# Kernel optimization log

Measured on AMD Instinct MI355X. Metric: run time of the kernel, lower is better.

## Reference

```python
import jax, jax.numpy as jnp
import numpy as np

N_NODES = 100000
N_EDGES = 1250000
D = 64
L = 2  # number of conv layers (len(hid_ds) - 1)
BN_EPS = 1e-5


def setup_inputs() -> dict:
    key = jax.random.key(0)
    ks = jax.random.split(key, 16)
    s = 1.0 / np.sqrt(D)
    inp = {
        "x": jax.random.normal(ks[0], (N_NODES, D), dtype=jnp.float32),
        "edge_index": jax.random.randint(ks[1], (2, N_EDGES), 0, N_NODES, dtype=jnp.int32),
        "batch": jnp.zeros((N_NODES,), dtype=jnp.int32),
        # stacked per-layer parameters [L, D, D] / [L, D]
        "Wk": jax.random.uniform(ks[2], (L, D, D), jnp.float32, -s, s),
        "bk": jax.random.uniform(ks[3], (L, D), jnp.float32, -s, s),
        "Wq": jax.random.uniform(ks[4], (L, D, D), jnp.float32, -s, s),
        "bq": jax.random.uniform(ks[5], (L, D), jnp.float32, -s, s),
        "Wv": jax.random.uniform(ks[6], (L, D, D), jnp.float32, -s, s),
        "bv": jax.random.uniform(ks[7], (L, D), jnp.float32, -s, s),
        "Ws": jax.random.uniform(ks[8], (L, D, D), jnp.float32, -s, s),
        "bs": jax.random.uniform(ks[9], (L, D), jnp.float32, -s, s),
        "bias": jnp.zeros((L, D), dtype=jnp.float32),
        "gamma": jnp.ones((L, D), dtype=jnp.float32),
        "beta": jnp.zeros((L, D), dtype=jnp.float32),
    }
    return inp


def _res_gated_conv(x, src, dst, Wk, bk, Wq, bq, Wv, bv, Ws, bs, b):
    # per-node linear transforms (dense GEMMs on [N, D])
    k = x @ Wk + bk          # applied at target i
    q = x @ Wq + bq          # applied at source j
    v = x @ Wv + bv          # message value from source j
    # edge-wise gather -> gate -> message: [E, D]
    msg = jax.nn.sigmoid(k[dst] + q[src]) * v[src]
    # scatter-add aggregation to targets
    agg = jnp.zeros_like(k).at[dst].add(msg)
    return agg + x @ Ws + bs + b


def _batch_norm(x, gamma, beta):
    # training-mode BatchNorm1d over node axis, biased variance
    mean = jnp.mean(x, axis=0)
    var = jnp.mean(jnp.square(x - mean), axis=0)
    return (x - mean) * jax.lax.rsqrt(var + BN_EPS) * gamma + beta


def reference(x, edge_index, batch, Wk, bk, Wq, bq, Wv, bv, Ws, bs, bias, gamma, beta):
    src = edge_index[0]  # source j
    dst = edge_index[1]  # target i
    for l in range(L):
        x = _res_gated_conv(x, src, dst, Wk[l], bk[l], Wq[l], bq[l],
                            Wv[l], bv[l], Ws[l], bs[l], bias[l])
        x = jax.nn.relu(x)
        x = _batch_norm(x, gamma[l], beta[l])
    return x
```

## Files before the change

### kernel.cpp

```cpp
#include <hip/hip_runtime.h>
#include <math.h>

#define D 64
#define BN_EPS 1e-5f
#define CH 160
#define BSH 7
#define BCAP 8192
#define NBLK 256

using short8 = __attribute__((ext_vector_type(8))) short;
using f32x4  = __attribute__((ext_vector_type(4))) float;

static __device__ __forceinline__ unsigned short f2bf(float f) {
    unsigned int u = __float_as_uint(f);
    unsigned int r = (u + 0x7fffu + ((u >> 16) & 1u)) >> 16;
    return (unsigned short)r;
}
static __device__ __forceinline__ float bf2f(unsigned short u) {
    return __uint_as_float(((unsigned int)u) << 16);
}
static __device__ __forceinline__ float clamp60(float x) {
    return fminf(fmaxf(x, -60.f), 60.f);
}

__global__ __launch_bounds__(256) void prep_weights(
    const float* __restrict__ Wk, const float* __restrict__ Wq,
    const float* __restrict__ Wv, const float* __restrict__ Ws,
    unsigned short* __restrict__ Wfrag)
{
    int idx = blockIdx.x * 256 + threadIdx.x;
    int i    = idx & 7;
    int lane = (idx >> 3) & 63;
    int kb   = (idx >> 9) & 1;
    int nc   = (idx >> 10) & 3;
    int m    = (idx >> 12) & 3;
    int l    = (idx >> 14) & 1;
    int k = kb * 32 + (lane >> 4) * 8 + i;
    int n = nc * 16 + (lane & 15);
    const float* W = (m == 0) ? Wk : (m == 1) ? Wq : (m == 2) ? Wv : Ws;
    Wfrag[idx] = f2bf(W[(size_t)l * 4096 + k * 64 + n]);
}

template<bool APPLY_BN>
__global__ __launch_bounds__(256) void gemm_fused(
    const float* x,
    const unsigned short* __restrict__ Wfrag,
    const float* __restrict__ bk, const float* __restrict__ bq,
    const float* __restrict__ bv, const float* __restrict__ bs,
    const float* __restrict__ bias, const float* __restrict__ stats,
    unsigned short* __restrict__ EKh, unsigned int* __restrict__ QV,
    float* AGG, int nrows)
{
    __shared__ unsigned short xt[64 * 64];
    const int t = threadIdx.x;
    const int row0 = blockIdx.x * 64;

    #pragma unroll
    for (int it = 0; it < 4; ++it) {
        int fidx = t + it * 256;
        int r = fidx >> 4, c4 = fidx & 15;
        int grow = row0 + r;
        float4 v = make_float4(0.f, 0.f, 0.f, 0.f);
        if (grow < nrows)
            v = *reinterpret_cast<const float4*>(&x[(size_t)grow * D + c4 * 4]);
        if (APPLY_BN) {
            const float4* st4 = reinterpret_cast<const float4*>(stats);
            float4 sc = st4[32 + c4], sh = st4[48 + c4];
            v.x = fmaxf(v.x, 0.f) * sc.x + sh.x;
            v.y = fmaxf(v.y, 0.f) * sc.y + sh.y;
            v.z = fmaxf(v.z, 0.f) * sc.z + sh.z;
            v.w = fmaxf(v.w, 0.f) * sc.w + sh.w;
        }
        ushort4 b;
        b.x = f2bf(v.x); b.y = f2bf(v.y); b.z = f2bf(v.z); b.w = f2bf(v.w);
        int phys = (c4 >> 1) ^ (r & 7);
        *reinterpret_cast<ushort4*>(&xt[r * 64 + phys * 8 + (c4 & 1) * 4]) = b;
    }
    __syncthreads();

    const int w = t >> 6, lane = t & 63;
    const int rbase = w * 16;

    short8 A[2];
    #pragma unroll
    for (int kb = 0; kb < 2; ++kb) {
        int r = rbase + (lane & 15);
        int c16 = (kb * 4 + (lane >> 4)) ^ (r & 7);
        A[kb] = *reinterpret_cast<const short8*>(&xt[r * 64 + c16 * 8]);
    }

    f32x4 acc[4][4];
    #pragma unroll
    for (int m = 0; m < 4; ++m)
        #pragma unroll
        for (int nc = 0; nc < 4; ++nc)
            acc[m][nc] = (f32x4){0.f, 0.f, 0.f, 0.f};

    #pragma unroll
    for (int nc = 0; nc < 4; ++nc) {
        #pragma unroll
        for (int m = 0; m < 4; ++m) {
            #pragma unroll
            for (int kb = 0; kb < 2; ++kb) {
                short8 B = *reinterpret_cast<const short8*>(
                    &Wfrag[((((m * 4 + nc) * 2 + kb) * 64) + lane) * 8]);
                acc[m][nc] = __builtin_amdgcn_mfma_f32_16x16x32_bf16(A[kb], B, acc[m][nc], 0, 0, 0);
            }
        }
    }

    const int crow = rbase + ((lane >> 4) << 2);
    #pragma unroll
    for (int nc = 0; nc < 4; ++nc) {
        int c = nc * 16 + (lane & 15);
        float bkc = bk[c], bqc = bq[c], bvc = bv[c], bsc = bs[c] + bias[c];
        #pragma unroll
        for (int reg = 0; reg < 4; ++reg) {
            int grow = row0 + crow + reg;
            if (grow < nrows) {
                size_t o = (size_t)grow * D + c;
                EKh[o] = f2bf(__expf(-clamp60(acc[0][nc][reg] + bkc)));
                float eq = __expf(-clamp60(acc[1][nc][reg] + bqc));
                QV[o] = ((unsigned int)f2bf(acc[2][nc][reg] + bvc) << 16) | (unsigned int)f2bf(eq);
                AGG[o] = acc[3][nc][reg] + bsc;
            }
        }
    }
}

__global__ __launch_bounds__(256) void bin_count(const int* __restrict__ dst,
                                                 int* __restrict__ cnt,
                                                 int nedges, int NB)
{
    __shared__ int h[1024];
    const int t = threadIdx.x, b = blockIdx.x;
    for (int i = t; i < NB; i += 256) h[i] = 0;
    __syncthreads();
    const int e0 = (int)(((long long)nedges * b) / NBLK);
    const int e1 = (int)(((long long)nedges * (b + 1)) / NBLK);
    for (int i = e0 + t; i < e1; i += 256)
        atomicAdd(&h[dst[i] >> BSH], 1);
    __syncthreads();
    for (int i = t; i < NB; i += 256) cnt[b * NB + i] = h[i];
}

__global__ __launch_bounds__(256) void scan_mat(const int* __restrict__ cnt,
                                                int* __restrict__ basel,
                                                int* __restrict__ btot, int NB)
{
    __shared__ int tmp[256];
    const int k = blockIdx.x;
    const int t = threadIdx.x;
    int v = cnt[t * NB + k];
    tmp[t] = v;
    __syncthreads();
    for (int off = 1; off < 256; off <<= 1) {
        int add = (t >= off) ? tmp[t - off] : 0;
        __syncthreads();
        tmp[t] += add;
        __syncthreads();
    }
    basel[t * NB + k] = tmp[t] - v;
    if (t == 255) btot[k] = tmp[255];
}

__global__ __launch_bounds__(1024) void scan_buckets(const int* __restrict__ btot,
                                                     int* __restrict__ boff,
                                                     float* __restrict__ stats,
                                                     int* __restrict__ offs,
                                                     int NB, int n, int nedges)
{
    __shared__ int tmp[1024];
    const int t = threadIdx.x;
    int v = (t < NB) ? btot[t] : 0;
    tmp[t] = v;
    __syncthreads();
    for (int off = 1; off < 1024; off <<= 1) {
        int add = (t >= off) ? tmp[t - off] : 0;
        __syncthreads();
        tmp[t] += add;
        __syncthreads();
    }
    if (t < NB) boff[t] = tmp[t] - v;
    if (t < 128) stats[t] = 0.f;
    if (t == 0) offs[n] = nedges;
}

__global__ __launch_bounds__(256) void bin_emit(const int* __restrict__ src,
                                                const int* __restrict__ dst,
                                                const int* __restrict__ basel,
                                                const int* __restrict__ boff,
                                                unsigned int* __restrict__ bin,
                                                int nedges, int NB)
{
    __shared__ int cur[1024];
    const int t = threadIdx.x, b = blockIdx.x;
    for (int i = t; i < NB; i += 256) cur[i] = boff[i] + basel[b * NB + i];
    __syncthreads();
    const int e0 = (int)(((long long)nedges * b) / NBLK);
    const int e1 = (int)(((long long)nedges * (b + 1)) / NBLK);
    for (int i = e0 + t; i < e1; i += 256) {
        int d = dst[i];
        int pos = atomicAdd(&cur[d >> BSH], 1);
        bin[pos] = ((unsigned int)src[i] << BSH) | (unsigned int)(d & ((1 << BSH) - 1));
    }
}

__global__ __launch_bounds__(256) void bucket_csr(const unsigned int* __restrict__ bin,
                                                  const int* __restrict__ boff,
                                                  const int* __restrict__ btot,
                                                  int* __restrict__ offs,
                                                  int* __restrict__ csr_src, int n)
{
    __shared__ unsigned int lsrc[BCAP];
    __shared__ int ldeg[128], loff[128], lcur[128];
    const int t = threadIdx.x;
    const int b = blockIdx.x;
    const int base = boff[b];
    const int cnt  = btot[b];

    if (t < 128) ldeg[t] = 0;
    __syncthreads();
    for (int j = t; j < cnt; j += 256)
        atomicAdd(&ldeg[bin[base + j] & ((1 << BSH) - 1)], 1);
    __syncthreads();
    if (t < 128) loff[t] = ldeg[t];
    __syncthreads();
    for (int off = 1; off < 128; off <<= 1) {
        int add = (t < 128 && t >= off) ? loff[t - off] : 0;
        __syncthreads();
        if (t < 128) loff[t] += add;
        __syncthreads();
    }
    if (t < 128) {
        int ex = loff[t] - ldeg[t];
        lcur[t] = ex;
        int node = (b << BSH) + t;
        if (node < n) offs[node] = base + ex;
    }
    __syncthreads();
    for (int j = t; j < cnt; j += 256) {
        unsigned int e = bin[base + j];
        int pos = atomicAdd(&lcur[e & ((1 << BSH) - 1)], 1);
        lsrc[pos] = e >> BSH;
    }
    __syncthreads();
    for (int j = t; j < cnt; j += 256)
        csr_src[base + j] = (int)lsrc[j];
}

__global__ __launch_bounds__(256) void nstart_bs(const int* __restrict__ offs,
                                                 int* __restrict__ node_start,
                                                 int n, int NC)
{
    int c = blockIdx.x * 256 + threadIdx.x;
    if (c >= NC) return;
    int target = c * CH;
    int a = 0, bnd = n;
    while (a < bnd) {
        int mid = (a + bnd) >> 1;
        if (offs[mid + 1] > target) bnd = mid; else a = mid + 1;
    }
    node_start[c] = a;
}

__global__ __launch_bounds__(256) void edge_agg(
    const int* __restrict__ csr_src, const int* __restrict__ offs,
    const int* __restrict__ node_start,
    const unsigned short* __restrict__ EKh, const unsigned int* __restrict__ QV,
    float* __restrict__ AGG, int nnodes)
{
    const int lane  = threadIdx.x & 63;
    const int chunk = __builtin_amdgcn_readfirstlane((int)((blockIdx.x * 256 + threadIdx.x) >> 6));
    const int Etot  = offs[nnodes];
    const int e0 = chunk * CH;
    if (e0 >= Etot) return;
    const int e1 = min(e0 + CH, Etot);

    int n      = node_start[chunk];
    int nstart = offs[n];
    int nend   = offs[n + 1];

    float acc = 0.f;
    float ek  = bf2f(EKh[((size_t)n << 6) | lane]);

    auto flush = [&](bool partial) {
        int idx = (n << 6) | lane;
        if (partial) atomicAdd(&AGG[idx], acc);
        else         AGG[idx] += acc;
    };
    auto advance = [&](int eidx) {
        do { ++n; } while (offs[n + 1] == eidx);
        nstart = eidx;
        nend   = offs[n + 1];
        acc = 0.f;
        ek  = bf2f(EKh[((size_t)n << 6) | lane]);
    };

    for (int e = e0; e < e1; e += 64) {
        const int cnt = min(64, e1 - e);
        int sAll = (lane < cnt) ? csr_src[e + lane] : 0;
        for (int b = 0; b < cnt; b += 16) {
            const int bc = min(16, cnt - b);
            unsigned int p[16];
            #pragma unroll
            for (int u = 0; u < 16; ++u) {
                if (u < bc) {
                    int s = __shfl(sAll, b + u);
                    p[u] = QV[((size_t)s << 6) | lane];
                }
            }
            #pragma unroll
            for (int u = 0; u < 16; ++u) {
                if (u < bc) {
                    int eidx = e + b + u;
                    if (eidx == nend) { flush(nstart < e0); advance(eidx); }
                    float eq = __uint_as_float(p[u] << 16);
                    float vv = __uint_as_float(p[u] & 0xffff0000u);
                    float g  = __builtin_amdgcn_rcpf(fmaf(ek, eq, 1.0f));
                    acc = fmaf(g, vv, acc);
                }
            }
        }
    }
    flush((nstart < e0) || (nend > e1));
}

__global__ __launch_bounds__(256) void relu_stats(
    const float* __restrict__ AGG, float* __restrict__ stats, int n4)
{
    __shared__ float ls[128];
    const int t = threadIdx.x;
    if (t < 128) ls[t] = 0.f;
    __syncthreads();
    int idx = blockIdx.x * 256 + t;
    const int stride = gridDim.x * 256;
    const int f0 = (idx << 2) & 63;
    float s0=0,s1=0,s2=0,s3=0,q0=0,q1=0,q2=0,q3=0;
    for (; idx < n4; idx += stride) {
        float4 a = reinterpret_cast<const float4*>(AGG)[idx];
        a.x = fmaxf(a.x, 0.f); a.y = fmaxf(a.y, 0.f);
        a.z = fmaxf(a.z, 0.f); a.w = fmaxf(a.w, 0.f);
        s0 += a.x; q0 = fmaf(a.x, a.x, q0);
        s1 += a.y; q1 = fmaf(a.y, a.y, q1);
        s2 += a.z; q2 = fmaf(a.z, a.z, q2);
        s3 += a.w; q3 = fmaf(a.w, a.w, q3);
    }
    atomicAdd(&ls[f0],     s0); atomicAdd(&ls[f0 + 1],     s1);
    atomicAdd(&ls[f0 + 2], s2); atomicAdd(&ls[f0 + 3],     s3);
    atomicAdd(&ls[64 + f0],     q0); atomicAdd(&ls[64 + f0 + 1], q1);
    atomicAdd(&ls[64 + f0 + 2], q2); atomicAdd(&ls[64 + f0 + 3], q3);
    __syncthreads();
    if (t < 128) atomicAdd(&stats[t], ls[t]);
}

__global__ void finalize_stats(float* __restrict__ stats,
                               const float* __restrict__ gamma,
                               const float* __restrict__ beta, int nrows)
{
    int t = threadIdx.x;
    float invN = 1.0f / (float)nrows;
    float mean = stats[t] * invN;
    float var  = stats[64 + t] * invN - mean * mean;
    float sc   = gamma[t] * rsqrtf(var + BN_EPS);
    stats[128 + t] = sc;
    stats[192 + t] = beta[t] - mean * sc;
    stats[t] = 0.f;
    stats[64 + t] = 0.f;
}

__global__ __launch_bounds__(256) void apply_bn(
    const float* __restrict__ AGG, const float* __restrict__ stats,
    float* __restrict__ xout, int ntot4)
{
    int idx = blockIdx.x * 256 + threadIdx.x;
    const int stride = gridDim.x * 256;
    const float4* st4 = reinterpret_cast<const float4*>(stats);
    for (; idx < ntot4; idx += stride) {
        float4 a = reinterpret_cast<const float4*>(AGG)[idx];
        int c4 = idx & 15;
        float4 sc = st4[32 + c4];
        float4 sh = st4[48 + c4];
        float4 o;
        o.x = fmaxf(a.x, 0.f) * sc.x + sh.x;
        o.y = fmaxf(a.y, 0.f) * sc.y + sh.y;
        o.z = fmaxf(a.z, 0.f) * sc.z + sh.z;
        o.w = fmaxf(a.w, 0.f) * sc.w + sh.w;
        reinterpret_cast<float4*>(xout)[idx] = o;
    }
}

extern "C" void kernel_launch(void* const* d_in, const int* in_sizes, int n_in,
                              void* d_out, int out_size, void* d_ws, size_t ws_size,
                              hipStream_t stream)
{
    const float* x     = (const float*)d_in[0];
    const int*   ei    = (const int*)d_in[1];
    const float* Wk    = (const float*)d_in[3];
    const float* bk    = (const float*)d_in[4];
    const float* Wq    = (const float*)d_in[5];
    const float* bq    = (const float*)d_in[6];
    const float* Wv    = (const float*)d_in[7];
    const float* bv    = (const float*)d_in[8];
    const float* Ws    = (const float*)d_in[9];
    const float* bs    = (const float*)d_in[10];
    const float* bias  = (const float*)d_in[11];
    const float* gamma = (const float*)d_in[12];
    const float* beta  = (const float*)d_in[13];

    const int nrows  = in_sizes[0] / D;
    const int nedges = in_sizes[1] / 2;
    const int nm     = nrows * D;
    const int NB     = (nrows + (1 << BSH) - 1) >> BSH;
    const int NC     = (nedges + CH - 1) / CH;

    float* out = (float*)d_out;
    float* ws  = (float*)d_ws;
    unsigned short* EKh = (unsigned short*)ws;
    unsigned int* QV = (unsigned int*)(EKh + nm);
    float* AGG = (float*)(QV + nm);
    float* stats = AGG + nm;
    int* offs    = (int*)(stats + 256);
    unsigned int* bin = (unsigned int*)(offs + nrows + 1);
    int* csr_src = (int*)(bin + nedges);
    int* cnt     = csr_src + nedges;
    int* basel   = cnt + NBLK * NB;
    int* btot    = basel + NBLK * NB;
    int* boff    = btot + NB;
    int* nstart_map = boff + NB;
    unsigned short* Wfrag = (unsigned short*)(nstart_map + NC);

    const int* srcI = ei;
    const int* dstI = ei + nedges;

    const int gemm_blocks = (nrows + 63) / 64;
    const int agg_blocks  = (NC + 3) / 4;

    prep_weights<<<128, 256, 0, stream>>>(Wk, Wq, Wv, Ws, Wfrag);
    bin_count<<<NBLK, 256, 0, stream>>>(dstI, cnt, nedges, NB);
    scan_mat<<<NB, 256, 0, stream>>>(cnt, basel, btot, NB);
    scan_buckets<<<1, 1024, 0, stream>>>(btot, boff, stats, offs, NB, nrows, nedges);
    bin_emit<<<NBLK, 256, 0, stream>>>(srcI, dstI, basel, boff, bin, nedges, NB);
    bucket_csr<<<NB, 256, 0, stream>>>(bin, boff, btot, offs, csr_src, nrows);
    nstart_bs<<<(NC + 255) / 256, 256, 0, stream>>>(offs, nstart_map, nrows, NC);

    gemm_fused<false><<<gemm_blocks, 256, 0, stream>>>(x, Wfrag,
        bk, bq, bv, bs, bias, stats, EKh, QV, AGG, nrows);
    edge_agg<<<agg_blocks, 256, 0, stream>>>(csr_src, offs, nstart_map, EKh, QV, AGG, nrows);
    relu_stats<<<1024, 256, 0, stream>>>(AGG, stats, nm / 4);
    finalize_stats<<<1, 64, 0, stream>>>(stats, gamma, beta, nrows);

    gemm_fused<true><<<gemm_blocks, 256, 0, stream>>>(AGG, Wfrag + 16384,
        bk + D, bq + D, bv + D, bs + D, bias + D, stats, EKh, QV, AGG, nrows);
    edge_agg<<<agg_blocks, 256, 0, stream>>>(csr_src, offs, nstart_map, EKh, QV, AGG, nrows);
    relu_stats<<<1024, 256, 0, stream>>>(AGG, stats, nm / 4);
    finalize_stats<<<1, 64, 0, stream>>>(stats, gamma + D, beta + D, nrows);
    apply_bn<<<2048, 256, 0, stream>>>(AGG, stats, out, nm / 4);
}
```

Baseline: 339.7 us.

## Fuse BN statistics into edge aggregation and fold finalize into consumers

Removes the separate relu_stats pass over AGG by accumulating ReLU sum and sum-of-squares in edge_agg when a node's row is fully owned by a wave. A new cleanup_stats kernel picks up nodes finished via atomics or with no incoming edges. The finalize_stats kernel is dropped: the next GEMM and apply_bn recompute scale and shift into shared memory. This saves a full read of AGG and a launch per layer, but adds cleanup logic and extra global atomics whose correctness depends on subtle chunk-boundary ownership.

```diff
diff --git a/kernel.cpp b/kernel.cpp
--- a/kernel.cpp
+++ b/kernel.cpp
@@ -48,12 +48,26 @@
     const float* __restrict__ bk, const float* __restrict__ bq,
     const float* __restrict__ bv, const float* __restrict__ bs,
     const float* __restrict__ bias, const float* __restrict__ stats,
+    const float* __restrict__ gamma, const float* __restrict__ beta,
     unsigned short* __restrict__ EKh, unsigned int* __restrict__ QV,
     float* AGG, int nrows)
 {
     __shared__ unsigned short xt[64 * 64];
+    __shared__ float scsh[128];
     const int t = threadIdx.x;
     const int row0 = blockIdx.x * 64;
+
+    if (APPLY_BN) {
+        if (t < 64) {
+            float invN = 1.0f / (float)nrows;
+            float mean = stats[t] * invN;
+            float var  = stats[64 + t] * invN - mean * mean;
+            float sc   = gamma[t] * rsqrtf(var + BN_EPS);
+            scsh[t] = sc;
+            scsh[64 + t] = beta[t] - mean * sc;
+        }
+        __syncthreads();
+    }
 
     #pragma unroll
     for (int it = 0; it < 4; ++it) {
@@ -64,8 +78,8 @@
         if (grow < nrows)
             v = *reinterpret_cast<const float4*>(&x[(size_t)grow * D + c4 * 4]);
         if (APPLY_BN) {
-            const float4* st4 = reinterpret_cast<const float4*>(stats);
-            float4 sc = st4[32 + c4], sh = st4[48 + c4];
+            float4 sc = reinterpret_cast<const float4*>(scsh)[c4];
+            float4 sh = reinterpret_cast<const float4*>(scsh)[16 + c4];
             v.x = fmaxf(v.x, 0.f) * sc.x + sh.x;
             v.y = fmaxf(v.y, 0.f) * sc.y + sh.y;
             v.z = fmaxf(v.z, 0.f) * sc.z + sh.z;
@@ -182,7 +196,7 @@
         __syncthreads();
     }
     if (t < NB) boff[t] = tmp[t] - v;
-    if (t < 128) stats[t] = 0.f;
+    if (t < 256) stats[t] = 0.f;
     if (t == 0) offs[n] = nedges;
 }
 
@@ -268,119 +282,153 @@
     const int* __restrict__ csr_src, const int* __restrict__ offs,
     const int* __restrict__ node_start,
     const unsigned short* __restrict__ EKh, const unsigned int* __restrict__ QV,
-    float* __restrict__ AGG, int nnodes)
-{
-    const int lane  = threadIdx.x & 63;
-    const int chunk = __builtin_amdgcn_readfirstlane((int)((blockIdx.x * 256 + threadIdx.x) >> 6));
+    float* __restrict__ AGG, float* __restrict__ stats, int nnodes)
+{
+    const int t = threadIdx.x;
+    const int lane  = t & 63;
+    const int chunk = __builtin_amdgcn_readfirstlane((int)((blockIdx.x * 256 + t) >> 6));
     const int Etot  = offs[nnodes];
     const int e0 = chunk * CH;
-    if (e0 >= Etot) return;
-    const int e1 = min(e0 + CH, Etot);
-
-    int n      = node_start[chunk];
-    int nstart = offs[n];
-    int nend   = offs[n + 1];
-
-    float acc = 0.f;
-    float ek  = bf2f(EKh[((size_t)n << 6) | lane]);
-
-    auto flush = [&](bool partial) {
-        int idx = (n << 6) | lane;
-        if (partial) atomicAdd(&AGG[idx], acc);
-        else         AGG[idx] += acc;
-    };
-    auto advance = [&](int eidx) {
-        do { ++n; } while (offs[n + 1] == eidx);
-        nstart = eidx;
-        nend   = offs[n + 1];
-        acc = 0.f;
-        ek  = bf2f(EKh[((size_t)n << 6) | lane]);
-    };
-
-    for (int e = e0; e < e1; e += 64) {
-        const int cnt = min(64, e1 - e);
-        int sAll = (lane < cnt) ? csr_src[e + lane] : 0;
-        for (int b = 0; b < cnt; b += 16) {
-            const int bc = min(16, cnt - b);
-            unsigned int p[16];
-            #pragma unroll
-            for (int u = 0; u < 16; ++u) {
-                if (u < bc) {
-                    int s = __shfl(sAll, b + u);
-                    p[u] = QV[((size_t)s << 6) | lane];
+    float lsum = 0.f, lsq = 0.f;
+
+    if (e0 < Etot) {
+        const int e1 = min(e0 + CH, Etot);
+
+        int n      = node_start[chunk];
+        int nstart = offs[n];
+        int nend   = offs[n + 1];
+
+        float acc = 0.f;
+        float ek  = bf2f(EKh[((size_t)n << 6) | lane]);
+
+        auto flush = [&](bool partial) {
+            int idx = (n << 6) | lane;
+            if (partial) {
+                atomicAdd(&AGG[idx], acc);
+            } else {
+                float cur = AGG[idx] + acc;
+                AGG[idx] = cur;
+                float y = fmaxf(cur, 0.f);
+                lsum += y;
+                lsq = fmaf(y, y, lsq);
+            }
+        };
+        auto advance = [&](int eidx) {
+            do { ++n; } while (offs[n + 1] == eidx);
+            nstart = eidx;
+            nend   = offs[n + 1];
+            acc = 0.f;
+            ek  = bf2f(EKh[((size_t)n << 6) | lane]);
+        };
+
+        for (int e = e0; e < e1; e += 64) {
+            const int cnt = min(64, e1 - e);
+            int sAll = (lane < cnt) ? csr_src[e + lane] : 0;
+            for (int b = 0; b < cnt; b += 16) {
+                const int bc = min(16, cnt - b);
+                unsigned int p[16];
+                #pragma unroll
+                for (int u = 0; u < 16; ++u) {
+                    if (u < bc) {
+                        int s = __shfl(sAll, b + u);
+                        p[u] = QV[((size_t)s << 6) | lane];
+                    }
+                }
+                #pragma unroll
+                for (int u = 0; u < 16; ++u) {
+                    if (u < bc) {
+                        int eidx = e + b + u;
+                        if (eidx == nend) { flush(nstart < e0); advance(eidx); }
+                        float eq = __uint_as_float(p[u] << 16);
+                        float vv = __uint_as_float(p[u] & 0xffff0000u);
+                        float g  = __builtin_amdgcn_rcpf(fmaf(ek, eq, 1.0f));
+                        acc = fmaf(g, vv, acc);
+                    }
                 }
             }
-            #pragma unroll
-            for (int u = 0; u < 16; ++u) {
-                if (u < bc) {
-                    int eidx = e + b + u;
-                    if (eidx == nend) { flush(nstart < e0); advance(eidx); }
-                    float eq = __uint_as_float(p[u] << 16);
-                    float vv = __uint_as_float(p[u] & 0xffff0000u);
-                    float g  = __builtin_amdgcn_rcpf(fmaf(ek, eq, 1.0f));
-                    acc = fmaf(g, vv, acc);
-                }
+        }
+        flush((nstart < e0) || (nend > e1));
+    }
+
+    __shared__ float ss[256], sq2[256];
+    ss[t] = lsum; sq2[t] = lsq;
+    __syncthreads();
+    if (t < 64) {
+        float s4 = ss[t] + ss[t + 64] + ss[t + 128] + ss[t + 192];
+        float q4 = sq2[t] + sq2[t + 64] + sq2[t + 128] + sq2[t + 192];
+        if (s4 != 0.f) atomicAdd(&stats[t], s4);
+        if (q4 != 0.f) atomicAdd(&stats[64 + t], q4);
+    }
+}
+
+__global__ __launch_bounds__(256) void cleanup_stats(
+    const int* __restrict__ offs, const int* __restrict__ node_start,
+    const float* __restrict__ AGG, float* __restrict__ stats, int n, int NC)
+{
+    const int t = threadIdx.x;
+    const int lane = t & 63;
+    const int wave = (blockIdx.x * 256 + t) >> 6;
+    float lsum = 0.f, lsq = 0.f;
+
+    if (wave < NC) {
+        int c = wave;
+        if (c > 0) {
+            int nd = node_start[c];
+            int s = offs[nd];
+            if (s < c * CH && s >= (c - 1) * CH) {
+                float y = fmaxf(AGG[((size_t)nd << 6) | lane], 0.f);
+                lsum = y; lsq = y * y;
             }
         }
-    }
-    flush((nstart < e0) || (nend > e1));
-}
-
-__global__ __launch_bounds__(256) void relu_stats(
-    const float* __restrict__ AGG, float* __restrict__ stats, int n4)
-{
-    __shared__ float ls[128];
-    const int t = threadIdx.x;
-    if (t < 128) ls[t] = 0.f;
-    __syncthreads();
+    } else {
+        int base = (wave - NC) << 6;
+        int nd = base + lane;
+        bool empty = (nd < n) && (offs[nd + 1] == offs[nd]);
+        unsigned long long mask = __ballot(empty);
+        while (mask) {
+            int b = __ffsll((unsigned long long)mask) - 1;
+            mask &= mask - 1;
+            int nd2 = base + b;
+            float y = fmaxf(AGG[((size_t)nd2 << 6) | lane], 0.f);
+            lsum += y; lsq = fmaf(y, y, lsq);
+        }
+    }
+
+    __shared__ float ss[256], sq2[256];
+    ss[t] = lsum; sq2[t] = lsq;
+    __syncthreads();
+    if (t < 64) {
+        float s4 = ss[t] + ss[t + 64] + ss[t + 128] + ss[t + 192];
+        float q4 = sq2[t] + sq2[t + 64] + sq2[t + 128] + sq2[t + 192];
+        if (s4 != 0.f) atomicAdd(&stats[t], s4);
+        if (q4 != 0.f) atomicAdd(&stats[64 + t], q4);
+    }
+}
+
+__global__ __launch_bounds__(256) void apply_bn(
+    const float* __restrict__ AGG, const float* __restrict__ stats,
+    const float* __restrict__ gamma, const float* __restrict__ beta,
+    float* __restrict__ xout, int ntot4, int nrows)
+{
+    __shared__ float scsh[128];
+    const int t = threadIdx.x;
+    if (t < 64) {
+        float invN = 1.0f / (float)nrows;
+        float mean = stats[t] * invN;
+        float var  = stats[64 + t] * invN - mean * mean;
+        float sc   = gamma[t] * rsqrtf(var + BN_EPS);
+        scsh[t] = sc;
+        scsh[64 + t] = beta[t] - mean * sc;
+    }
+    __syncthreads();
+
     int idx = blockIdx.x * 256 + t;
     const int stride = gridDim.x * 256;
-    const int f0 = (idx << 2) & 63;
-    float s0=0,s1=0,s2=0,s3=0,q0=0,q1=0,q2=0,q3=0;
-    for (; idx < n4; idx += stride) {
-        float4 a = reinterpret_cast<const float4*>(AGG)[idx];
-        a.x = fmaxf(a.x, 0.f); a.y = fmaxf(a.y, 0.f);
-        a.z = fmaxf(a.z, 0.f); a.w = fmaxf(a.w, 0.f);
-        s0 += a.x; q0 = fmaf(a.x, a.x, q0);
-        s1 += a.y; q1 = fmaf(a.y, a.y, q1);
-        s2 += a.z; q2 = fmaf(a.z, a.z, q2);
-        s3 += a.w; q3 = fmaf(a.w, a.w, q3);
-    }
-    atomicAdd(&ls[f0],     s0); atomicAdd(&ls[f0 + 1],     s1);
-    atomicAdd(&ls[f0 + 2], s2); atomicAdd(&ls[f0 + 3],     s3);
-    atomicAdd(&ls[64 + f0],     q0); atomicAdd(&ls[64 + f0 + 1], q1);
-    atomicAdd(&ls[64 + f0 + 2], q2); atomicAdd(&ls[64 + f0 + 3], q3);
-    __syncthreads();
-    if (t < 128) atomicAdd(&stats[t], ls[t]);
-}
-
-__global__ void finalize_stats(float* __restrict__ stats,
-                               const float* __restrict__ gamma,
-                               const float* __restrict__ beta, int nrows)
-{
-    int t = threadIdx.x;
-    float invN = 1.0f / (float)nrows;
-    float mean = stats[t] * invN;
-    float var  = stats[64 + t] * invN - mean * mean;
-    float sc   = gamma[t] * rsqrtf(var + BN_EPS);
-    stats[128 + t] = sc;
-    stats[192 + t] = beta[t] - mean * sc;
-    stats[t] = 0.f;
-    stats[64 + t] = 0.f;
-}
-
-__global__ __launch_bounds__(256) void apply_bn(
-    const float* __restrict__ AGG, const float* __restrict__ stats,
-    float* __restrict__ xout, int ntot4)
-{
-    int idx = blockIdx.x * 256 + threadIdx.x;
-    const int stride = gridDim.x * 256;
-    const float4* st4 = reinterpret_cast<const float4*>(stats);
     for (; idx < ntot4; idx += stride) {
         float4 a = reinterpret_cast<const float4*>(AGG)[idx];
         int c4 = idx & 15;
-        float4 sc = st4[32 + c4];
-        float4 sh = st4[48 + c4];
+        float4 sc = reinterpret_cast<const float4*>(scsh)[c4];
+        float4 sh = reinterpret_cast<const float4*>(scsh)[16 + c4];
         float4 o;
         o.x = fmaxf(a.x, 0.f) * sc.x + sh.x;
         o.y = fmaxf(a.y, 0.f) * sc.y + sh.y;
@@ -435,6 +483,8 @@
 
     const int gemm_blocks = (nrows + 63) / 64;
     const int agg_blocks  = (NC + 3) / 4;
+    const int clean_waves = NC + (nrows + 63) / 64;
+    const int clean_blocks = (clean_waves + 3) / 4;
 
     prep_weights<<<128, 256, 0, stream>>>(Wk, Wq, Wv, Ws, Wfrag);
     bin_count<<<NBLK, 256, 0, stream>>>(dstI, cnt, nedges, NB);
@@ -445,15 +495,13 @@
     nstart_bs<<<(NC + 255) / 256, 256, 0, stream>>>(offs, nstart_map, nrows, NC);
 
     gemm_fused<false><<<gemm_blocks, 256, 0, stream>>>(x, Wfrag,
-        bk, bq, bv, bs, bias, stats, EKh, QV, AGG, nrows);
-    edge_agg<<<agg_blocks, 256, 0, stream>>>(csr_src, offs, nstart_map, EKh, QV, AGG, nrows);
-    relu_stats<<<1024, 256, 0, stream>>>(AGG, stats, nm / 4);
-    finalize_stats<<<1, 64, 0, stream>>>(stats, gamma, beta, nrows);
+        bk, bq, bv, bs, bias, stats, gamma, beta, EKh, QV, AGG, nrows);
+    edge_agg<<<agg_blocks, 256, 0, stream>>>(csr_src, offs, nstart_map, EKh, QV, AGG, stats, nrows);
+    cleanup_stats<<<clean_blocks, 256, 0, stream>>>(offs, nstart_map, AGG, stats, nrows, NC);
 
     gemm_fused<true><<<gemm_blocks, 256, 0, stream>>>(AGG, Wfrag + 16384,
-        bk + D, bq + D, bv + D, bs + D, bias + D, stats, EKh, QV, AGG, nrows);
-    edge_agg<<<agg_blocks, 256, 0, stream>>>(csr_src, offs, nstart_map, EKh, QV, AGG, nrows);
-    relu_stats<<<1024, 256, 0, stream>>>(AGG, stats, nm / 4);
-    finalize_stats<<<1, 64, 0, stream>>>(stats, gamma + D, beta + D, nrows);
-    apply_bn<<<2048, 256, 0, stream>>>(AGG, stats, out, nm / 4);
-}
+        bk + D, bq + D, bv + D, bs + D, bias + D, stats, gamma, beta, EKh, QV, AGG, nrows);
+    edge_agg<<<agg_blocks, 256, 0, stream>>>(csr_src, offs, nstart_map, EKh, QV, AGG, stats + 128, nrows);
+    cleanup_stats<<<clean_blocks, 256, 0, stream>>>(offs, nstart_map, AGG, stats + 128, nrows, NC);
+    apply_bn<<<2048, 256, 0, stream>>>(AGG, stats + 128, gamma + D, beta + D, out, nm / 4, nrows);
+}
```

After: 448.8 us. 1.32x slower.
